# Kernel tuning notes

Hardware: AMD Instinct MI355X
Metric: run time of the kernel (lower is better)

The kernel has to match this reference:

```python
import jax, jax.numpy as jnp
import numpy as np

D = 1024
H = 16
HD = D // H
SCALE = HD ** -0.5


def setup_inputs() -> dict:
    key = jax.random.key(0)
    ks = jax.random.split(key, 6)
    B, S = 2, 2048
    lim = np.sqrt(6.0 / (D + D))  # xavier uniform for square weights
    query = jax.random.normal(ks[0], (B, S, D), dtype=jnp.float32)
    Wq = jax.random.uniform(ks[1], (D, D), jnp.float32, -lim, lim)
    Wk = jax.random.uniform(ks[2], (D, D), jnp.float32, -lim, lim)
    Wv = jax.random.uniform(ks[3], (D, D), jnp.float32, -lim, lim)
    Wo = jax.random.uniform(ks[4], (D, D), jnp.float32, -lim, lim)
    bq = jnp.zeros((D,), jnp.float32)
    bk = jnp.zeros((D,), jnp.float32)
    bv = jnp.zeros((D,), jnp.float32)
    bo = jnp.zeros((D,), jnp.float32)
    # causal mask: True = masked (strictly upper triangular)
    attn_mask = jnp.triu(jnp.ones((S, S), dtype=bool), k=1)
    return {"query": query, "Wq": Wq, "bq": bq, "Wk": Wk, "bk": bk,
            "Wv": Wv, "bv": bv, "Wo": Wo, "bo": bo, "attn_mask": attn_mask}


def reference(query, Wq, bq, Wk, bk, Wv, bv, Wo, bo, attn_mask):
    B, Sq, _ = query.shape
    # projections (torch Linear: x @ W.T + b); self-attention (key=value=query)
    q = (query @ Wq.T + bq).reshape(B, Sq, H, HD).transpose(0, 2, 1, 3)  # [B,H,Sq,hd]
    k = (query @ Wk.T + bk).reshape(B, Sq, H, HD).transpose(0, 2, 1, 3)
    v = (query @ Wv.T + bv).reshape(B, Sq, H, HD).transpose(0, 2, 1, 3)
    scores = jnp.einsum('bhqd,bhkd->bhqk', q, k) * SCALE
    scores = jnp.where(attn_mask[None, None, :, :], -jnp.inf, scores)
    weights = jax.nn.softmax(scores, axis=-1)  # dropout p=0.0 -> identity
    out = jnp.einsum('bhqk,bhkd->bhqd', weights, v)
    out = out.transpose(0, 2, 1, 3).reshape(B, Sq, D)
    output = out @ Wo.T + bo
    return output, weights
```

## Files before the change

kernel.cpp:

```cpp
#include <hip/hip_runtime.h>
#include <hip/hip_bf16.h>
#include <stdint.h>

#define DMODEL 1024
#define NH     16
#define HDIM   64
#define BATCH  2
#define SEQ    2048
#define NROWS  (BATCH*SEQ)
#define NBH    (BATCH*NH)
#define SCALE  0.125f

typedef unsigned short u16;
typedef __bf16 bf16x8 __attribute__((ext_vector_type(8)));
typedef float  f32x4  __attribute__((ext_vector_type(4)));

#define MFMA(a,b,c) __builtin_amdgcn_mfma_f32_16x16x32_bf16((a),(b),(c),0,0,0)
#define BAR() __builtin_amdgcn_s_barrier()
#define WAITVM(N) asm volatile("s_waitcnt vmcnt(" #N ")" ::: "memory")

__device__ __forceinline__ u16 f2bf(float f) {
  union { float f; uint32_t u; } v; v.f = f;
  return (u16)((v.u + 0x7fffu + ((v.u >> 16) & 1u)) >> 16);
}

__device__ __forceinline__ void gl16(const void* g, void* l) {
  __builtin_amdgcn_global_load_lds((const __attribute__((address_space(1))) void*)g,
                                   (__attribute__((address_space(3))) void*)l,
                                   16, 0, 0);
}

#define LDF(arr, r, ch) (*(const bf16x8*)(&(arr)[(((r) << 6)) + ((((ch) ^ ((r) & 7))) << 3)]))
#define LDV(r, ch)      (*(const bf16x8*)(&lv [(((r) << 7)) + ((((ch) ^ ((r) & 7))) << 3)]))

#define XCH   (NROWS*DMODEL/4)
#define WCH   (DMODEL*DMODEL/4)
__global__ void cvt_all(const float* __restrict__ x,  const float* __restrict__ Wq,
                        const float* __restrict__ Wk, const float* __restrict__ Wv,
                        const float* __restrict__ Wo,
                        u16* __restrict__ Xb, u16* __restrict__ Wqb, u16* __restrict__ Wkb,
                        u16* __restrict__ Wvb, u16* __restrict__ Wob)
{
  int g = blockIdx.x * 256 + threadIdx.x;
  const float* src; u16* dst; int off;
  if (g < XCH) { src = x; dst = Xb; off = g * 4; }
  else {
    int t = g - XCH; int w = t >> 18; off = (t & (WCH - 1)) * 4;
    src = (w == 0) ? Wq : (w == 1) ? Wk : (w == 2) ? Wv : Wo;
    dst = (w == 0) ? Wqb : (w == 1) ? Wkb : (w == 2) ? Wvb : Wob;
  }
  float4 f = *(const float4*)(src + off);
  ushort4 o;
  o.x = f2bf(f.x); o.y = f2bf(f.y); o.z = f2bf(f.z); o.w = f2bf(f.w);
  *(ushort4*)(dst + off) = o;
}

__launch_bounds__(256, 2)
__global__ void qkv_proj(const u16* __restrict__ Xb,
                         const u16* __restrict__ Wqb,
                         const u16* __restrict__ Wkb,
                         const u16* __restrict__ Wvb,
                         const float* __restrict__ bqp,
                         const float* __restrict__ bkp,
                         const float* __restrict__ bvp,
                         u16* __restrict__ qb, u16* __restrict__ kb, u16* __restrict__ vtb)
{
  __shared__ __attribute__((aligned(16))) u16 la[2][128 * 64];
  __shared__ __attribute__((aligned(16))) u16 lb[2][128 * 64];
  const int tid  = threadIdx.x;
  const int lane = tid & 63, wave = tid >> 6;
  const int quad = lane >> 4, lm = lane & 15;

  int flat = blockIdx.y * 32 + blockIdx.x;
  int jj = flat >> 3;
  const int m0 = ((flat & 7) * 4 + (jj & 3)) * 128;
  const int ct = jj >> 2;
  const int proj = ct >> 3;
  const int n0 = (ct & 7) * 128;
  const u16*  W    = (proj == 0) ? Wqb : (proj == 1) ? Wkb : Wvb;
  const float* bias = (proj == 0) ? bqp : (proj == 1) ? bkp : bvp;

  const int sr = tid >> 3, sch = tid & 7;

  const f32x4 fzero = {0.f, 0.f, 0.f, 0.f};
  f32x4 acc[4][4];
#pragma unroll
  for (int i = 0; i < 4; i++)
#pragma unroll
    for (int j = 0; j < 4; j++) acc[i][j] = fzero;

  const int wm0 = (wave & 1) * 64, wn0 = (wave >> 1) * 64;

#pragma unroll
  for (int i = 0; i < 4; i++) {
    int r = sr + i * 32;
    int cs = (sch ^ (r & 7)) << 3;
    gl16(Xb + (size_t)(m0 + r) * DMODEL + cs, &la[0][(wave * 64 + i * 256) << 3]);
    gl16(W  + (size_t)(n0 + r) * DMODEL + cs, &lb[0][(wave * 64 + i * 256) << 3]);
  }

  for (int s = 0; s < DMODEL / 64; s++) {
    int cur = s & 1;
    if (s < DMODEL / 64 - 1) {
      int k0 = (s + 1) * 64;
#pragma unroll
      for (int i = 0; i < 4; i++) {
        int r = sr + i * 32;
        int cs = (sch ^ (r & 7)) << 3;
        gl16(Xb + (size_t)(m0 + r) * DMODEL + k0 + cs, &la[cur ^ 1][(wave * 64 + i * 256) << 3]);
        gl16(W  + (size_t)(n0 + r) * DMODEL + k0 + cs, &lb[cur ^ 1][(wave * 64 + i * 256) << 3]);
      }
      WAITVM(8);
    } else {
      WAITVM(0);
    }
    BAR();
#pragma unroll
    for (int ks = 0; ks < 2; ks++) {
      bf16x8 af[4], bfg[4];
#pragma unroll
      for (int i = 0; i < 4; i++) af[i]  = LDF(la[cur], wm0 + i * 16 + lm, ks * 4 + quad);
#pragma unroll
      for (int j = 0; j < 4; j++) bfg[j] = LDF(lb[cur], wn0 + j * 16 + lm, ks * 4 + quad);
#pragma unroll
      for (int i = 0; i < 4; i++)
#pragma unroll
        for (int j = 0; j < 4; j++)
          acc[i][j] = MFMA(af[i], bfg[j], acc[i][j]);
    }
    BAR();
  }

#pragma unroll
  for (int j = 0; j < 4; j++) {
    int o = n0 + wn0 + j * 16 + lm;
    float bs = bias[o];
    int h = o >> 6, hd = o & 63;
#pragma unroll
    for (int i = 0; i < 4; i++) {
      int m = m0 + wm0 + i * 16 + quad * 4;
      int b = m >> 11, ss = m & (SEQ - 1);
      if (proj == 2) {
        ushort4 ov;
        ov.x = f2bf(acc[i][j][0] + bs); ov.y = f2bf(acc[i][j][1] + bs);
        ov.z = f2bf(acc[i][j][2] + bs); ov.w = f2bf(acc[i][j][3] + bs);
        *(ushort4*)(vtb + (((size_t)(b * NH + h)) * HDIM + hd) * SEQ + ss) = ov;
      } else {
        u16* dst = (proj == 0) ? qb : kb;
#pragma unroll
        for (int r = 0; r < 4; r++)
          dst[(((size_t)(b * NH + h)) * SEQ + ss + r) * HDIM + hd] = f2bf(acc[i][j][r] + bs);
      }
    }
  }
}

__launch_bounds__(256, 2)
__global__ void attn_fused(const u16* __restrict__ qb, const u16* __restrict__ kb,
                           const u16* __restrict__ vtb,
                           float* __restrict__ wts, u16* __restrict__ ctxb)
{
  __shared__ __attribute__((aligned(16))) u16 lk[2][128 * 64];
  __shared__ __attribute__((aligned(16))) u16 lv[64 * 128];
  __shared__ __attribute__((aligned(16))) u16 lp[4][16 * 128];

  const int tid  = threadIdx.x;
  const int lane = tid & 63, wave = tid >> 6;
  const int quad = lane >> 4, lm = lane & 15;

  int flat = blockIdx.y * 16 + blockIdx.x;
  int wk = (flat & 7) * 64 + (flat >> 3);
  const int bh = wk >> 4;
  const int bx = wk & 15;
  const int b = bh >> 4, hh = bh & 15;
  u16* lpw = lp[wave];

  const u16* Qb = qb  + (size_t)bh * SEQ * HDIM;
  const u16* K  = kb  + (size_t)bh * SEQ * HDIM;
  const u16* Vt = vtb + (size_t)bh * HDIM * SEQ;

  const f32x4 fzero = {0.f, 0.f, 0.f, 0.f};
  const int kr0 = tid >> 3, kch = tid & 7;
  const int vr0 = tid >> 4, vch = tid & 15;

#pragma unroll 1
  for (int sp = 0; sp < 2; sp++) {
    const int qt = sp ? (31 - bx) : bx;
    const int ktmax = qt >> 1;
    const int qg = qt * 64 + wave * 16 + lm;
    float* Wr = wts + ((size_t)bh * SEQ + qt * 64) * SEQ;

    bf16x8 qreg0 = *(const bf16x8*)(Qb + (size_t)(qt * 64 + wave * 16 + lm) * HDIM + (quad << 3));
    bf16x8 qreg1 = *(const bf16x8*)(Qb + (size_t)(qt * 64 + wave * 16 + lm) * HDIM + 32 + (quad << 3));

    float lsum = 0.f;
#pragma unroll
    for (int i = 0; i < 4; i++) {
      int r = kr0 + i * 32;
      gl16(K + (size_t)r * HDIM + ((kch ^ (r & 7)) << 3), &lk[0][(wave * 64 + i * 256) << 3]);
    }
#pragma unroll 1
    for (int kt = 0; kt <= ktmax; kt++) {
      int cur = kt & 1;
      if (kt < ktmax) {
#pragma unroll
        for (int i = 0; i < 4; i++) {
          int r = kr0 + i * 32;
          gl16(K + (size_t)((kt + 1) * 128 + r) * HDIM + ((kch ^ (r & 7)) << 3),
               &lk[cur ^ 1][(wave * 64 + i * 256) << 3]);
        }
        WAITVM(4);
      } else {
        WAITVM(0);
      }
      BAR();
      f32x4 s[8];
#pragma unroll
      for (int t = 0; t < 8; t++) s[t] = fzero;
#pragma unroll
      for (int t = 0; t < 8; t++) {
        int rr = t * 16 + lm;
        s[t] = MFMA(LDF(lk[cur], rr, quad),     qreg0, s[t]);
        s[t] = MFMA(LDF(lk[cur], rr, 4 + quad), qreg1, s[t]);
      }
#pragma unroll
      for (int t = 0; t < 8; t++)
#pragma unroll
        for (int r = 0; r < 4; r++) {
          int kc = kt * 128 + t * 16 + quad * 4 + r;
          lsum += (kc <= qg) ? __expf(s[t][r] * SCALE) : 0.f;
        }
      BAR();
    }
    lsum += __shfl_xor(lsum, 16);
    lsum += __shfl_xor(lsum, 32);
    const float linv = 1.f / lsum;

    f32x4 acc_o[4];
#pragma unroll
    for (int dt = 0; dt < 4; dt++) acc_o[dt] = fzero;

#pragma unroll
    for (int i = 0; i < 4; i++) {
      int r = kr0 + i * 32;
      gl16(K + (size_t)r * HDIM + ((kch ^ (r & 7)) << 3), &lk[0][(wave * 64 + i * 256) << 3]);
    }
#pragma unroll 1
    for (int kt = 0; kt <= ktmax; kt++) {
      int cur = kt & 1;
      if (kt < ktmax) {
#pragma unroll
        for (int i = 0; i < 4; i++) {
          int r = kr0 + i * 32;
          gl16(K + (size_t)((kt + 1) * 128 + r) * HDIM + ((kch ^ (r & 7)) << 3),
               &lk[cur ^ 1][(wave * 64 + i * 256) << 3]);
        }
      }
#pragma unroll
      for (int i = 0; i < 4; i++) {
        int r = vr0 + i * 16;
        gl16(Vt + (size_t)r * SEQ + kt * 128 + ((vch ^ (r & 7)) << 3),
             &lv[(wave * 64 + i * 256) << 3]);
      }
      if (kt < ktmax) { WAITVM(8); } else { WAITVM(4); }
      BAR();

      f32x4 s[8];
#pragma unroll
      for (int t = 0; t < 8; t++) s[t] = fzero;
#pragma unroll
      for (int t = 0; t < 8; t++) {
        int rr = t * 16 + lm;
        s[t] = MFMA(LDF(lk[cur], rr, quad),     qreg0, s[t]);
        s[t] = MFMA(LDF(lk[cur], rr, 4 + quad), qreg1, s[t]);
      }

#pragma unroll
      for (int t = 0; t < 8; t++) {
        f32x4 pv;
#pragma unroll
        for (int r = 0; r < 4; r++) {
          int kc = kt * 128 + t * 16 + quad * 4 + r;
          float p = __expf(s[t][r] * SCALE) * linv;
          pv[r] = (kc <= qg) ? p : 0.f;
        }
        *(f32x4*)(Wr + (size_t)(wave * 16 + lm) * SEQ + kt * 128 + t * 16 + quad * 4) = pv;
        ushort4 pb4;
        pb4.x = f2bf(pv[0]); pb4.y = f2bf(pv[1]); pb4.z = f2bf(pv[2]); pb4.w = f2bf(pv[3]);
        int c8 = (t * 4 + quad) ^ ((lm & 7) << 1);
        *(ushort4*)(lpw + lm * 128 + (c8 << 2)) = pb4;
      }

      WAITVM(8);
      BAR();

#pragma unroll
      for (int ks = 0; ks < 4; ks++) {
        int c8r = (ks * 8 + quad * 2) ^ ((lm & 7) << 1);
        bf16x8 pb = *(const bf16x8*)(lpw + lm * 128 + (c8r << 2));
#pragma unroll
        for (int dt = 0; dt < 4; dt++) {
          bf16x8 a = LDV(dt * 16 + lm, ks * 4 + quad);
          acc_o[dt] = MFMA(a, pb, acc_o[dt]);
        }
      }
      BAR();
    }

    const int kz = (ktmax + 1) * 128;
    if (kz < SEQ) {
#pragma unroll
      for (int rg = 0; rg < 4; rg++) {
        float* rp = Wr + (size_t)(wave * 16 + rg * 4 + quad) * SEQ;
        for (int c = kz + lm * 4; c < SEQ; c += 64)
          *(f32x4*)(rp + c) = fzero;
      }
    }

    {
      int q = qt * 64 + wave * 16 + lm;
      u16* cp = ctxb + ((size_t)(b * SEQ + q)) * DMODEL + hh * HDIM;
#pragma unroll
      for (int dt = 0; dt < 4; dt++) {
        ushort4 o;
        o.x = f2bf(acc_o[dt][0]); o.y = f2bf(acc_o[dt][1]);
        o.z = f2bf(acc_o[dt][2]); o.w = f2bf(acc_o[dt][3]);
        *(ushort4*)(cp + dt * 16 + quad * 4) = o;
      }
    }
  }
}

__launch_bounds__(256, 2)
__global__ void out_proj(const u16* __restrict__ ctxb, const u16* __restrict__ Wob,
                         const float* __restrict__ bop, float* __restrict__ out)
{
  __shared__ __attribute__((aligned(16))) u16 la[2][128 * 64];
  __shared__ __attribute__((aligned(16))) u16 lb[2][128 * 64];
  const int tid  = threadIdx.x;
  const int lane = tid & 63, wave = tid >> 6;
  const int quad = lane >> 4, lm = lane & 15;

  int flat = blockIdx.y * 32 + blockIdx.x;
  int jj = flat >> 3;
  const int m0 = ((flat & 7) * 4 + (jj & 3)) * 128;
  const int n0 = (jj >> 2) * 128;

  const int sr = tid >> 3, sch = tid & 7;

  const f32x4 fzero = {0.f, 0.f, 0.f, 0.f};
  f32x4 acc[4][4];
#pragma unroll
  for (int i = 0; i < 4; i++)
#pragma unroll
    for (int j = 0; j < 4; j++) acc[i][j] = fzero;

  const int wm0 = (wave & 1) * 64, wn0 = (wave >> 1) * 64;

#pragma unroll
  for (int i = 0; i < 4; i++) {
    int r = sr + i * 32;
    int cs = (sch ^ (r & 7)) << 3;
    gl16(ctxb + (size_t)(m0 + r) * DMODEL + cs, &la[0][(wave * 64 + i * 256) << 3]);
    gl16(Wob  + (size_t)(n0 + r) * DMODEL + cs, &lb[0][(wave * 64 + i * 256) << 3]);
  }

  for (int s = 0; s < DMODEL / 64; s++) {
    int cur = s & 1;
    if (s < DMODEL / 64 - 1) {
      int k0 = (s + 1) * 64;
#pragma unroll
      for (int i = 0; i < 4; i++) {
        int r = sr + i * 32;
        int cs = (sch ^ (r & 7)) << 3;
        gl16(ctxb + (size_t)(m0 + r) * DMODEL + k0 + cs, &la[cur ^ 1][(wave * 64 + i * 256) << 3]);
        gl16(Wob  + (size_t)(n0 + r) * DMODEL + k0 + cs, &lb[cur ^ 1][(wave * 64 + i * 256) << 3]);
      }
      WAITVM(8);
    } else {
      WAITVM(0);
    }
    BAR();
#pragma unroll
    for (int ks = 0; ks < 2; ks++) {
      bf16x8 af[4], bfg[4];
#pragma unroll
      for (int i = 0; i < 4; i++) af[i]  = LDF(la[cur], wm0 + i * 16 + lm, ks * 4 + quad);
#pragma unroll
      for (int j = 0; j < 4; j++) bfg[j] = LDF(lb[cur], wn0 + j * 16 + lm, ks * 4 + quad);
#pragma unroll
      for (int i = 0; i < 4; i++)
#pragma unroll
        for (int j = 0; j < 4; j++)
          acc[i][j] = MFMA(af[i], bfg[j], acc[i][j]);
    }
    BAR();
  }

#pragma unroll
  for (int j = 0; j < 4; j++) {
    int o = n0 + wn0 + j * 16 + lm;
    float bs = bop[o];
#pragma unroll
    for (int i = 0; i < 4; i++)
#pragma unroll
      for (int r = 0; r < 4; r++) {
        int m = m0 + wm0 + i * 16 + quad * 4 + r;
        out[(size_t)m * DMODEL + o] = acc[i][j][r] + bs;
      }
  }
}

extern "C" void kernel_launch(void* const* d_in, const int* in_sizes, int n_in,
                              void* d_out, int out_size, void* d_ws, size_t ws_size,
                              hipStream_t stream)
{
  (void)in_sizes; (void)n_in; (void)out_size; (void)ws_size;
  const float* x  = (const float*)d_in[0];
  const float* Wq = (const float*)d_in[1];
  const float* bq = (const float*)d_in[2];
  const float* Wk = (const float*)d_in[3];
  const float* bk = (const float*)d_in[4];
  const float* Wv = (const float*)d_in[5];
  const float* bv = (const float*)d_in[6];
  const float* Wo = (const float*)d_in[7];
  const float* bo = (const float*)d_in[8];

  float* out = (float*)d_out;
  float* wts = out + (size_t)NROWS * DMODEL;

  u16* Xb   = (u16*)d_ws;
  u16* Wqb  = Xb   + (size_t)NROWS * DMODEL;
  u16* Wkb  = Wqb  + (size_t)DMODEL * DMODEL;
  u16* Wvb  = Wkb  + (size_t)DMODEL * DMODEL;
  u16* Wob  = Wvb  + (size_t)DMODEL * DMODEL;
  u16* qb   = Wob  + (size_t)DMODEL * DMODEL;
  u16* kb   = qb   + (size_t)NROWS * DMODEL;
  u16* vtb  = kb   + (size_t)NROWS * DMODEL;
  u16* ctxb = vtb  + (size_t)NROWS * DMODEL;

  cvt_all<<<(XCH + 4 * WCH) / 256, 256, 0, stream>>>(x, Wq, Wk, Wv, Wo,
                                                     Xb, Wqb, Wkb, Wvb, Wob);
  qkv_proj<<<dim3(NROWS / 128, 24), 256, 0, stream>>>(Xb, Wqb, Wkb, Wvb, bq, bk, bv, qb, kb, vtb);
  attn_fused<<<dim3(16, NBH), 256, 0, stream>>>(qb, kb, vtb, wts, ctxb);
  out_proj<<<dim3(NROWS / 128, DMODEL / 128), 256, 0, stream>>>(ctxb, Wob, bo, out);
}
```

Before: 680.2 us.

## Drop LDS double buffering to raise occupancy and split attention blocks per query tile

Removes the double-buffered LDS staging in both GEMM kernels and the attention kernel, so each tile is loaded and waited on synchronously. Less shared memory per block allows raising launch bounds to 3 blocks per CU. Attention now launches 1024 blocks, one per query tile in longest-first order, instead of 512 blocks each handling a balanced pair of tiles. It also adds s_setprio around MFMA sections. The trade is higher occupancy against losing in-block load/compute overlap and the pairwise load balance.

```diff
diff --git a/kernel.cpp b/kernel.cpp
--- a/kernel.cpp
+++ b/kernel.cpp
@@ -55,7 +55,7 @@
   *(ushort4*)(dst + off) = o;
 }
 
-__launch_bounds__(256, 2)
+__launch_bounds__(256, 3)
 __global__ void qkv_proj(const u16* __restrict__ Xb,
                          const u16* __restrict__ Wqb,
                          const u16* __restrict__ Wkb,
@@ -65,8 +65,8 @@
                          const float* __restrict__ bvp,
                          u16* __restrict__ qb, u16* __restrict__ kb, u16* __restrict__ vtb)
 {
-  __shared__ __attribute__((aligned(16))) u16 la[2][128 * 64];
-  __shared__ __attribute__((aligned(16))) u16 lb[2][128 * 64];
+  __shared__ __attribute__((aligned(16))) u16 la[128 * 64];
+  __shared__ __attribute__((aligned(16))) u16 lb[128 * 64];
   const int tid  = threadIdx.x;
   const int lane = tid & 63, wave = tid >> 6;
   const int quad = lane >> 4, lm = lane & 15;
@@ -91,37 +91,23 @@
 
   const int wm0 = (wave & 1) * 64, wn0 = (wave >> 1) * 64;
 
-#pragma unroll
-  for (int i = 0; i < 4; i++) {
-    int r = sr + i * 32;
-    int cs = (sch ^ (r & 7)) << 3;
-    gl16(Xb + (size_t)(m0 + r) * DMODEL + cs, &la[0][(wave * 64 + i * 256) << 3]);
-    gl16(W  + (size_t)(n0 + r) * DMODEL + cs, &lb[0][(wave * 64 + i * 256) << 3]);
-  }
-
-  for (int s = 0; s < DMODEL / 64; s++) {
-    int cur = s & 1;
-    if (s < DMODEL / 64 - 1) {
-      int k0 = (s + 1) * 64;
-#pragma unroll
-      for (int i = 0; i < 4; i++) {
-        int r = sr + i * 32;
-        int cs = (sch ^ (r & 7)) << 3;
-        gl16(Xb + (size_t)(m0 + r) * DMODEL + k0 + cs, &la[cur ^ 1][(wave * 64 + i * 256) << 3]);
-        gl16(W  + (size_t)(n0 + r) * DMODEL + k0 + cs, &lb[cur ^ 1][(wave * 64 + i * 256) << 3]);
-      }
-      WAITVM(8);
-    } else {
-      WAITVM(0);
-    }
+  for (int k0 = 0; k0 < DMODEL; k0 += 64) {
+#pragma unroll
+    for (int i = 0; i < 4; i++) {
+      int r = sr + i * 32;
+      int cs = (sch ^ (r & 7)) << 3;
+      gl16(Xb + (size_t)(m0 + r) * DMODEL + k0 + cs, &la[(wave * 64 + i * 256) << 3]);
+      gl16(W  + (size_t)(n0 + r) * DMODEL + k0 + cs, &lb[(wave * 64 + i * 256) << 3]);
+    }
+    WAITVM(0);
     BAR();
 #pragma unroll
     for (int ks = 0; ks < 2; ks++) {
       bf16x8 af[4], bfg[4];
 #pragma unroll
-      for (int i = 0; i < 4; i++) af[i]  = LDF(la[cur], wm0 + i * 16 + lm, ks * 4 + quad);
-#pragma unroll
-      for (int j = 0; j < 4; j++) bfg[j] = LDF(lb[cur], wn0 + j * 16 + lm, ks * 4 + quad);
+      for (int i = 0; i < 4; i++) af[i]  = LDF(la, wm0 + i * 16 + lm, ks * 4 + quad);
+#pragma unroll
+      for (int j = 0; j < 4; j++) bfg[j] = LDF(lb, wn0 + j * 16 + lm, ks * 4 + quad);
 #pragma unroll
       for (int i = 0; i < 4; i++)
 #pragma unroll
@@ -155,12 +141,12 @@
   }
 }
 
-__launch_bounds__(256, 2)
+__launch_bounds__(256, 3)
 __global__ void attn_fused(const u16* __restrict__ qb, const u16* __restrict__ kb,
                            const u16* __restrict__ vtb,
                            float* __restrict__ wts, u16* __restrict__ ctxb)
 {
-  __shared__ __attribute__((aligned(16))) u16 lk[2][128 * 64];
+  __shared__ __attribute__((aligned(16))) u16 lk[128 * 64];
   __shared__ __attribute__((aligned(16))) u16 lv[64 * 128];
   __shared__ __attribute__((aligned(16))) u16 lp[4][16 * 128];
 
@@ -168,10 +154,10 @@
   const int lane = tid & 63, wave = tid >> 6;
   const int quad = lane >> 4, lm = lane & 15;
 
-  int flat = blockIdx.y * 16 + blockIdx.x;
-  int wk = (flat & 7) * 64 + (flat >> 3);
-  const int bh = wk >> 4;
-  const int bx = wk & 15;
+  int flat = blockIdx.x;
+  int wk = (flat & 7) * 128 + (flat >> 3);
+  const int bh = wk >> 5;
+  const int qt = 31 - (wk & 31);
   const int b = bh >> 4, hh = bh & 15;
   u16* lpw = lp[wave];
 
@@ -183,160 +169,141 @@
   const int kr0 = tid >> 3, kch = tid & 7;
   const int vr0 = tid >> 4, vch = tid & 15;
 
+  const int ktmax = qt >> 1;
+  const int qg = qt * 64 + wave * 16 + lm;
+  float* Wr = wts + ((size_t)bh * SEQ + qt * 64) * SEQ;
+
+  bf16x8 qreg0 = *(const bf16x8*)(Qb + (size_t)(qt * 64 + wave * 16 + lm) * HDIM + (quad << 3));
+  bf16x8 qreg1 = *(const bf16x8*)(Qb + (size_t)(qt * 64 + wave * 16 + lm) * HDIM + 32 + (quad << 3));
+
+  float lsum = 0.f;
 #pragma unroll 1
-  for (int sp = 0; sp < 2; sp++) {
-    const int qt = sp ? (31 - bx) : bx;
-    const int ktmax = qt >> 1;
-    const int qg = qt * 64 + wave * 16 + lm;
-    float* Wr = wts + ((size_t)bh * SEQ + qt * 64) * SEQ;
-
-    bf16x8 qreg0 = *(const bf16x8*)(Qb + (size_t)(qt * 64 + wave * 16 + lm) * HDIM + (quad << 3));
-    bf16x8 qreg1 = *(const bf16x8*)(Qb + (size_t)(qt * 64 + wave * 16 + lm) * HDIM + 32 + (quad << 3));
-
-    float lsum = 0.f;
+  for (int kt = 0; kt <= ktmax; kt++) {
 #pragma unroll
     for (int i = 0; i < 4; i++) {
       int r = kr0 + i * 32;
-      gl16(K + (size_t)r * HDIM + ((kch ^ (r & 7)) << 3), &lk[0][(wave * 64 + i * 256) << 3]);
-    }
+      gl16(K + (size_t)(kt * 128 + r) * HDIM + ((kch ^ (r & 7)) << 3),
+           &lk[(wave * 64 + i * 256) << 3]);
+    }
+    WAITVM(0);
+    BAR();
+    f32x4 s[8];
+#pragma unroll
+    for (int t = 0; t < 8; t++) s[t] = fzero;
+    __builtin_amdgcn_s_setprio(1);
+#pragma unroll
+    for (int t = 0; t < 8; t++) {
+      int rr = t * 16 + lm;
+      s[t] = MFMA(LDF(lk, rr, quad),     qreg0, s[t]);
+      s[t] = MFMA(LDF(lk, rr, 4 + quad), qreg1, s[t]);
+    }
+    __builtin_amdgcn_s_setprio(0);
+#pragma unroll
+    for (int t = 0; t < 8; t++)
+#pragma unroll
+      for (int r = 0; r < 4; r++) {
+        int kc = kt * 128 + t * 16 + quad * 4 + r;
+        lsum += (kc <= qg) ? __expf(s[t][r] * SCALE) : 0.f;
+      }
+    BAR();
+  }
+  lsum += __shfl_xor(lsum, 16);
+  lsum += __shfl_xor(lsum, 32);
+  const float linv = 1.f / lsum;
+
+  f32x4 acc_o[4];
+#pragma unroll
+  for (int dt = 0; dt < 4; dt++) acc_o[dt] = fzero;
+
 #pragma unroll 1
-    for (int kt = 0; kt <= ktmax; kt++) {
-      int cur = kt & 1;
-      if (kt < ktmax) {
-#pragma unroll
-        for (int i = 0; i < 4; i++) {
-          int r = kr0 + i * 32;
-          gl16(K + (size_t)((kt + 1) * 128 + r) * HDIM + ((kch ^ (r & 7)) << 3),
-               &lk[cur ^ 1][(wave * 64 + i * 256) << 3]);
-        }
-        WAITVM(4);
-      } else {
-        WAITVM(0);
+  for (int kt = 0; kt <= ktmax; kt++) {
+#pragma unroll
+    for (int i = 0; i < 4; i++) {
+      int r = kr0 + i * 32;
+      gl16(K + (size_t)(kt * 128 + r) * HDIM + ((kch ^ (r & 7)) << 3),
+           &lk[(wave * 64 + i * 256) << 3]);
+    }
+#pragma unroll
+    for (int i = 0; i < 4; i++) {
+      int r = vr0 + i * 16;
+      gl16(Vt + (size_t)r * SEQ + kt * 128 + ((vch ^ (r & 7)) << 3),
+           &lv[(wave * 64 + i * 256) << 3]);
+    }
+    WAITVM(0);
+    BAR();
+
+    f32x4 s[8];
+#pragma unroll
+    for (int t = 0; t < 8; t++) s[t] = fzero;
+    __builtin_amdgcn_s_setprio(1);
+#pragma unroll
+    for (int t = 0; t < 8; t++) {
+      int rr = t * 16 + lm;
+      s[t] = MFMA(LDF(lk, rr, quad),     qreg0, s[t]);
+      s[t] = MFMA(LDF(lk, rr, 4 + quad), qreg1, s[t]);
+    }
+    __builtin_amdgcn_s_setprio(0);
+
+#pragma unroll
+    for (int t = 0; t < 8; t++) {
+      f32x4 pv;
+#pragma unroll
+      for (int r = 0; r < 4; r++) {
+        int kc = kt * 128 + t * 16 + quad * 4 + r;
+        float p = __expf(s[t][r] * SCALE) * linv;
+        pv[r] = (kc <= qg) ? p : 0.f;
       }
-      BAR();
-      f32x4 s[8];
-#pragma unroll
-      for (int t = 0; t < 8; t++) s[t] = fzero;
-#pragma unroll
-      for (int t = 0; t < 8; t++) {
-        int rr = t * 16 + lm;
-        s[t] = MFMA(LDF(lk[cur], rr, quad),     qreg0, s[t]);
-        s[t] = MFMA(LDF(lk[cur], rr, 4 + quad), qreg1, s[t]);
+      *(f32x4*)(Wr + (size_t)(wave * 16 + lm) * SEQ + kt * 128 + t * 16 + quad * 4) = pv;
+      ushort4 pb4;
+      pb4.x = f2bf(pv[0]); pb4.y = f2bf(pv[1]); pb4.z = f2bf(pv[2]); pb4.w = f2bf(pv[3]);
+      int c8 = (t * 4 + quad) ^ ((lm & 7) << 1);
+      *(ushort4*)(lpw + lm * 128 + (c8 << 2)) = pb4;
+    }
+
+    __builtin_amdgcn_s_setprio(1);
+#pragma unroll
+    for (int ks = 0; ks < 4; ks++) {
+      int c8r = (ks * 8 + quad * 2) ^ ((lm & 7) << 1);
+      bf16x8 pb = *(const bf16x8*)(lpw + lm * 128 + (c8r << 2));
+#pragma unroll
+      for (int dt = 0; dt < 4; dt++) {
+        bf16x8 a = LDV(dt * 16 + lm, ks * 4 + quad);
+        acc_o[dt] = MFMA(a, pb, acc_o[dt]);
       }
-#pragma unroll
-      for (int t = 0; t < 8; t++)
-#pragma unroll
-        for (int r = 0; r < 4; r++) {
-          int kc = kt * 128 + t * 16 + quad * 4 + r;
-          lsum += (kc <= qg) ? __expf(s[t][r] * SCALE) : 0.f;
-        }
-      BAR();
-    }
-    lsum += __shfl_xor(lsum, 16);
-    lsum += __shfl_xor(lsum, 32);
-    const float linv = 1.f / lsum;
-
-    f32x4 acc_o[4];
-#pragma unroll
-    for (int dt = 0; dt < 4; dt++) acc_o[dt] = fzero;
-
-#pragma unroll
-    for (int i = 0; i < 4; i++) {
-      int r = kr0 + i * 32;
-      gl16(K + (size_t)r * HDIM + ((kch ^ (r & 7)) << 3), &lk[0][(wave * 64 + i * 256) << 3]);
-    }
-#pragma unroll 1
-    for (int kt = 0; kt <= ktmax; kt++) {
-      int cur = kt & 1;
-      if (kt < ktmax) {
-#pragma unroll
-        for (int i = 0; i < 4; i++) {
-          int r = kr0 + i * 32;
-          gl16(K + (size_t)((kt + 1) * 128 + r) * HDIM + ((kch ^ (r & 7)) << 3),
-               &lk[cur ^ 1][(wave * 64 + i * 256) << 3]);
-        }
-      }
-#pragma unroll
-      for (int i = 0; i < 4; i++) {
-        int r = vr0 + i * 16;
-        gl16(Vt + (size_t)r * SEQ + kt * 128 + ((vch ^ (r & 7)) << 3),
-             &lv[(wave * 64 + i * 256) << 3]);
-      }
-      if (kt < ktmax) { WAITVM(8); } else { WAITVM(4); }
-      BAR();
-
-      f32x4 s[8];
-#pragma unroll
-      for (int t = 0; t < 8; t++) s[t] = fzero;
-#pragma unroll
-      for (int t = 0; t < 8; t++) {
-        int rr = t * 16 + lm;
-        s[t] = MFMA(LDF(lk[cur], rr, quad),     qreg0, s[t]);
-        s[t] = MFMA(LDF(lk[cur], rr, 4 + quad), qreg1, s[t]);
-      }
-
-#pragma unroll
-      for (int t = 0; t < 8; t++) {
-        f32x4 pv;
-#pragma unroll
-        for (int r = 0; r < 4; r++) {
-          int kc = kt * 128 + t * 16 + quad * 4 + r;
-          float p = __expf(s[t][r] * SCALE) * linv;
-          pv[r] = (kc <= qg) ? p : 0.f;
-        }
-        *(f32x4*)(Wr + (size_t)(wave * 16 + lm) * SEQ + kt * 128 + t * 16 + quad * 4) = pv;
-        ushort4 pb4;
-        pb4.x = f2bf(pv[0]); pb4.y = f2bf(pv[1]); pb4.z = f2bf(pv[2]); pb4.w = f2bf(pv[3]);
-        int c8 = (t * 4 + quad) ^ ((lm & 7) << 1);
-        *(ushort4*)(lpw + lm * 128 + (c8 << 2)) = pb4;
-      }
-
-      WAITVM(8);
-      BAR();
-
-#pragma unroll
-      for (int ks = 0; ks < 4; ks++) {
-        int c8r = (ks * 8 + quad * 2) ^ ((lm & 7) << 1);
-        bf16x8 pb = *(const bf16x8*)(lpw + lm * 128 + (c8r << 2));
-#pragma unroll
-        for (int dt = 0; dt < 4; dt++) {
-          bf16x8 a = LDV(dt * 16 + lm, ks * 4 + quad);
-          acc_o[dt] = MFMA(a, pb, acc_o[dt]);
-        }
-      }
-      BAR();
-    }
-
-    const int kz = (ktmax + 1) * 128;
-    if (kz < SEQ) {
-#pragma unroll
-      for (int rg = 0; rg < 4; rg++) {
-        float* rp = Wr + (size_t)(wave * 16 + rg * 4 + quad) * SEQ;
-        for (int c = kz + lm * 4; c < SEQ; c += 64)
-          *(f32x4*)(rp + c) = fzero;
-      }
-    }
-
-    {
-      int q = qt * 64 + wave * 16 + lm;
-      u16* cp = ctxb + ((size_t)(b * SEQ + q)) * DMODEL + hh * HDIM;
-#pragma unroll
-      for (int dt = 0; dt < 4; dt++) {
-        ushort4 o;
-        o.x = f2bf(acc_o[dt][0]); o.y = f2bf(acc_o[dt][1]);
-        o.z = f2bf(acc_o[dt][2]); o.w = f2bf(acc_o[dt][3]);
-        *(ushort4*)(cp + dt * 16 + quad * 4) = o;
-      }
-    }
-  }
-}
-
-__launch_bounds__(256, 2)
+    }
+    __builtin_amdgcn_s_setprio(0);
+    BAR();
+  }
+
+  const int kz = (ktmax + 1) * 128;
+  if (kz < SEQ) {
+#pragma unroll
+    for (int rg = 0; rg < 4; rg++) {
+      float* rp = Wr + (size_t)(wave * 16 + rg * 4 + quad) * SEQ;
+      for (int c = kz + lm * 4; c < SEQ; c += 64)
+        *(f32x4*)(rp + c) = fzero;
+    }
+  }
+
+  {
+    int q = qt * 64 + wave * 16 + lm;
+    u16* cp = ctxb + ((size_t)(b * SEQ + q)) * DMODEL + hh * HDIM;
+#pragma unroll
+    for (int dt = 0; dt < 4; dt++) {
+      ushort4 o;
+      o.x = f2bf(acc_o[dt][0]); o.y = f2bf(acc_o[dt][1]);
+      o.z = f2bf(acc_o[dt][2]); o.w = f2bf(acc_o[dt][3]);
+      *(ushort4*)(cp + dt * 16 + quad * 4) = o;
+    }
+  }
+}
+
+__launch_bounds__(256, 3)
 __global__ void out_proj(const u16* __restrict__ ctxb, const u16* __restrict__ Wob,
                          const float* __restrict__ bop, float* __restrict__ out)
 {
-  __shared__ __attribute__((aligned(16))) u16 la[2][128 * 64];
-  __shared__ __attribute__((aligned(16))) u16 lb[2][128 * 64];
+  __shared__ __attribute__((aligned(16))) u16 la[128 * 64];
+  __shared__ __attribute__((aligned(16))) u16 lb[128 * 64];
   const int tid  = threadIdx.x;
   const int lane = tid & 63, wave = tid >> 6;
   const int quad = lane >> 4, lm = lane & 15;
@@ -357,37 +324,23 @@
 
   const int wm0 = (wave & 1) * 64, wn0 = (wave >> 1) * 64;
 
-#pragma unroll
-  for (int i = 0; i < 4; i++) {
-    int r = sr + i * 32;
-    int cs = (sch ^ (r & 7)) << 3;
-    gl16(ctxb + (size_t)(m0 + r) * DMODEL + cs, &la[0][(wave * 64 + i * 256) << 3]);
-    gl16(Wob  + (size_t)(n0 + r) * DMODEL + cs, &lb[0][(wave * 64 + i * 256) << 3]);
-  }
-
-  for (int s = 0; s < DMODEL / 64; s++) {
-    int cur = s & 1;
-    if (s < DMODEL / 64 - 1) {
-      int k0 = (s + 1) * 64;
-#pragma unroll
-      for (int i = 0; i < 4; i++) {
-        int r = sr + i * 32;
-        int cs = (sch ^ (r & 7)) << 3;
-        gl16(ctxb + (size_t)(m0 + r) * DMODEL + k0 + cs, &la[cur ^ 1][(wave * 64 + i * 256) << 3]);
-        gl16(Wob  + (size_t)(n0 + r) * DMODEL + k0 + cs, &lb[cur ^ 1][(wave * 64 + i * 256) << 3]);
-      }
-      WAITVM(8);
-    } else {
-      WAITVM(0);
-    }
+  for (int k0 = 0; k0 < DMODEL; k0 += 64) {
+#pragma unroll
+    for (int i = 0; i < 4; i++) {
+      int r = sr + i * 32;
+      int cs = (sch ^ (r & 7)) << 3;
+      gl16(ctxb + (size_t)(m0 + r) * DMODEL + k0 + cs, &la[(wave * 64 + i * 256) << 3]);
+      gl16(Wob  + (size_t)(n0 + r) * DMODEL + k0 + cs, &lb[(wave * 64 + i * 256) << 3]);
+    }
+    WAITVM(0);
     BAR();
 #pragma unroll
     for (int ks = 0; ks < 2; ks++) {
       bf16x8 af[4], bfg[4];
 #pragma unroll
-      for (int i = 0; i < 4; i++) af[i]  = LDF(la[cur], wm0 + i * 16 + lm, ks * 4 + quad);
-#pragma unroll
-      for (int j = 0; j < 4; j++) bfg[j] = LDF(lb[cur], wn0 + j * 16 + lm, ks * 4 + quad);
+      for (int i = 0; i < 4; i++) af[i]  = LDF(la, wm0 + i * 16 + lm, ks * 4 + quad);
+#pragma unroll
+      for (int j = 0; j < 4; j++) bfg[j] = LDF(lb, wn0 + j * 16 + lm, ks * 4 + quad);
 #pragma unroll
       for (int i = 0; i < 4; i++)
 #pragma unroll
@@ -442,6 +395,6 @@
   cvt_all<<<(XCH + 4 * WCH) / 256, 256, 0, stream>>>(x, Wq, Wk, Wv, Wo,
                                                      Xb, Wqb, Wkb, Wvb, Wob);
   qkv_proj<<<dim3(NROWS / 128, 24), 256, 0, stream>>>(Xb, Wqb, Wkb, Wvb, bq, bk, bv, qb, kb, vtb);
-  attn_fused<<<dim3(16, NBH), 256, 0, stream>>>(qb, kb, vtb, wts, ctxb);
+  attn_fused<<<1024, 256, 0, stream>>>(qb, kb, vtb, wts, ctxb);
   out_proj<<<dim3(NROWS / 128, DMODEL / 128), 256, 0, stream>>>(ctxb, Wob, bo, out);
 }
```

Measured after the change: 680.1 us. Within noise of the previous version (-0.0%).
